# Optimization experiments

Measured on AMD Instinct MI355X. Metric: run time of the kernel, lower is better.

The kernel has to match this reference:

```python
import jax, jax.numpy as jnp
import numpy as np

NUM_HEADS = 8
EPS_OT = 0.05    # self.eps
BETA_T = 1.0     # self.beta_t
N_ITERS = 100    # Sinkhorn max_iter (reference runs all iterations; torch breaks early on convergence)


def setup_inputs() -> dict:
    key = jax.random.key(0)
    ks = jax.random.split(key, 10)
    B, N1, N2 = 16, 256, 576
    dim_t, dim_v, dim_out = 512, 512, 512
    s = 0.02  # conv1d k=1 init scale (stand-in for torch default init)
    f32 = jnp.float32
    return {
        "F_t": jax.random.normal(ks[0], (B, N1, dim_t), f32),
        "F_s": jax.random.normal(ks[1], (B, N2, dim_v), f32),
        # Conv1d(kernel_size=1) weights, squeezed to [out, in]; biases default-on in nn.Conv1d
        "Wq": jax.random.normal(ks[2], (dim_out, dim_t), f32) * s,
        "bq": jnp.zeros((dim_out,), f32),
        "Wk": jax.random.normal(ks[3], (dim_out, dim_v), f32) * s,
        "bk": jnp.zeros((dim_out,), f32),
        "Wv": jax.random.normal(ks[4], (dim_out, dim_v), f32) * s,
        "bv": jnp.zeros((dim_out,), f32),
        "Wp": jax.random.normal(ks[5], (dim_out, dim_out), f32) * s,
        "bp": jnp.zeros((dim_out,), f32),
    }


def sinkhorn_log_exp_sum(C, log_mu, log_nu, eps):
    # C: [BH, N1, N2]; fixed-length log-domain Sinkhorn.
    BH, N1, N2 = C.shape
    u0 = jnp.zeros((BH, N1), C.dtype)
    v0 = jnp.zeros((BH, N2), C.dtype)

    def body(carry, _):
        u, v = carry
        # single K per iteration; both u and v updates use the OLD (u, v), matching torch code
        K = (-C + u[:, :, None] + v[:, None, :]) / eps
        u_new = eps * (log_mu - jax.scipy.special.logsumexp(K, axis=2)) + u
        v_new = eps * (log_nu - jax.scipy.special.logsumexp(K, axis=1)) + v
        return (u_new, v_new), None

    (u, v), _ = jax.lax.scan(jax.checkpoint(body), (u0, v0), None, length=N_ITERS)
    return jnp.exp((-C + u[:, :, None] + v[:, None, :]) / eps)


def _l2norm(x, eps=1e-12):
    return x / jnp.maximum(jnp.linalg.norm(x, axis=-1, keepdims=True), eps)


def reference(F_t, F_s, Wq, bq, Wk, bk, Wv, bv, Wp, bp):
    B, N1, _ = F_t.shape
    N2 = F_s.shape[1]
    H = NUM_HEADS
    dim_out = Wq.shape[0]
    hd = dim_out // H

    # Conv1d(kernel=1) == pointwise linear over channel dim
    q = (F_t @ Wq.T + bq).reshape(B, N1, H, hd)
    k = (F_s @ Wk.T + bk).reshape(B, N2, H, hd)
    v = (F_s @ Wv.T + bv).reshape(B, N2, H, hd)

    q = _l2norm(q)
    k = _l2norm(k)

    sim = jnp.einsum('bnkc,bmkc->bknm', q, k) * BETA_T  # [B,H,N1,N2]
    wdist = (1.0 - sim).reshape(B * H, N1, N2)
    sim_f = sim.reshape(B * H, N1, N2)

    log_mu = jnp.log(jnp.asarray(1.0 / N1 + 1e-8, sim.dtype))
    log_nu = jnp.log(jnp.asarray(1.0 / N2 + 1e-8, sim.dtype))
    T = sinkhorn_log_exp_sum(wdist, log_mu, log_nu, EPS_OT)

    score_map = (N1 * N2 * sim_f * T).reshape(B, H, N1, N2)  # attn_drop = identity (p=0)
    F_t_a = jnp.einsum('bknm,bmkc->bnkc', score_map, v).reshape(B, N1, dim_out)
    F_t_a = F_t_a @ Wp.T + bp
    # torch: F_t_a / F_t_a.norm(dim=-1, keepdim=True)  (plain division, no eps clamp)
    F_t_a = F_t_a / jnp.linalg.norm(F_t_a, axis=-1, keepdims=True)
    return F_t_a  # proj_drop = identity (p=0)
```

## Files before the change

kernel.cpp:

```cpp
#include <hip/hip_runtime.h>
#include <math.h>

#define EPS_OT 0.05f
#define INV_EPS 20.0f

typedef unsigned short ushort_t;
typedef __attribute__((ext_vector_type(8))) short short8;
typedef __attribute__((ext_vector_type(4))) float f32x4;
union Pk { uint4 u; short8 s; };

__device__ __forceinline__ unsigned int f2bf(float f) {
  unsigned int u = __float_as_uint(f);
  return (u + 0x7FFFu + ((u >> 16) & 1u)) >> 16;
}
__device__ __forceinline__ float bf2f(unsigned int u) { return __uint_as_float(u << 16); }

__device__ __forceinline__ void bar_lds() {
  asm volatile("s_waitcnt lgkmcnt(0)" ::: "memory");
  __builtin_amdgcn_s_barrier();
  asm volatile("" ::: "memory");
}

__global__ __launch_bounds__(256) void pack_k(const float* __restrict__ F_t,
                                              const float* __restrict__ F_s,
                                              const float* __restrict__ Wq,
                                              const float* __restrict__ Wk,
                                              const float* __restrict__ Wv,
                                              const float* __restrict__ Wp,
                                              ushort_t* __restrict__ Fth, ushort_t* __restrict__ Ftl,
                                              ushort_t* __restrict__ Fsh, ushort_t* __restrict__ Fsl,
                                              ushort_t* __restrict__ Wqh, ushort_t* __restrict__ Wql,
                                              ushort_t* __restrict__ Wkh, ushort_t* __restrict__ Wkl,
                                              ushort_t* __restrict__ Wvh, ushort_t* __restrict__ Wvl,
                                              ushort_t* __restrict__ Wph) {
  const int blk = blockIdx.x;
  const float* src; ushort_t* dh; ushort_t* dl; size_t off;
  if (blk < 2048)      { src = F_t; dh = Fth; dl = Ftl; off = (size_t)blk * 1024; }
  else if (blk < 6656) { src = F_s; dh = Fsh; dl = Fsl; off = (size_t)(blk - 2048) * 1024; }
  else if (blk < 6912) { src = Wq;  dh = Wqh; dl = Wql; off = (size_t)(blk - 6656) * 1024; }
  else if (blk < 7168) { src = Wk;  dh = Wkh; dl = Wkl; off = (size_t)(blk - 6912) * 1024; }
  else if (blk < 7424) { src = Wv;  dh = Wvh; dl = Wvl; off = (size_t)(blk - 7168) * 1024; }
  else                 { src = Wp;  dh = Wph; dl = nullptr; off = (size_t)(blk - 7424) * 1024; }
  const size_t i = off + (size_t)threadIdx.x * 4;
  float4 f = *(const float4*)(src + i);
  unsigned int h0 = f2bf(f.x), h1 = f2bf(f.y), h2 = f2bf(f.z), h3 = f2bf(f.w);
  uint2 hh; hh.x = h0 | (h1 << 16); hh.y = h2 | (h3 << 16);
  *(uint2*)(dh + i) = hh;
  if (dl) {
    uint2 ll;
    ll.x = f2bf(f.x - bf2f(h0)) | (f2bf(f.y - bf2f(h1)) << 16);
    ll.y = f2bf(f.z - bf2f(h2)) | (f2bf(f.w - bf2f(h3)) << 16);
    *(uint2*)(dl + i) = ll;
  }
}

#define GEMM_HL_BODY()                                                                      \
  f32x4 acc[4] = {};                                                                        \
  for (int k0 = 0; k0 < 512; k0 += 64) {                                                    \
    uint4 a0 = *(const uint4*)(Xp_h + k0), a1 = *(const uint4*)(Xp_h + k0 + 8);             \
    uint4 b0 = *(const uint4*)(Xp_l + k0), b1 = *(const uint4*)(Xp_l + k0 + 8);             \
    uint4 c0 = *(const uint4*)(Wp_h + k0), c1 = *(const uint4*)(Wp_h + k0 + 8);             \
    uint4 d0 = *(const uint4*)(Wp_l + k0), d1 = *(const uint4*)(Wp_l + k0 + 8);             \
    __syncthreads();                                                                        \
    *(uint4*)&Xh[r][cg * 16] = a0; *(uint4*)&Xh[r][cg * 16 + 8] = a1;                       \
    *(uint4*)&Xl[r][cg * 16] = b0; *(uint4*)&Xl[r][cg * 16 + 8] = b1;                       \
    *(uint4*)&Wh[r][cg * 16] = c0; *(uint4*)&Wh[r][cg * 16 + 8] = c1;                       \
    *(uint4*)&Wl[r][cg * 16] = d0; *(uint4*)&Wl[r][cg * 16 + 8] = d1;                       \
    __syncthreads();                                                                        \
    _Pragma("unroll") for (int kst = 0; kst < 2; ++kst) {                                   \
      short8 ah = *(const short8*)&Xh[16 * w + li][kst * 32 + 8 * lg];                      \
      short8 al = *(const short8*)&Xl[16 * w + li][kst * 32 + 8 * lg];                      \
      _Pragma("unroll") for (int nt = 0; nt < 4; ++nt) {                                    \
        short8 bh = *(const short8*)&Wh[nt * 16 + li][kst * 32 + 8 * lg];                   \
        short8 bl = *(const short8*)&Wl[nt * 16 + li][kst * 32 + 8 * lg];                   \
        acc[nt] = __builtin_amdgcn_mfma_f32_16x16x32_bf16(ah, bh, acc[nt], 0, 0, 0);        \
        acc[nt] = __builtin_amdgcn_mfma_f32_16x16x32_bf16(ah, bl, acc[nt], 0, 0, 0);        \
        acc[nt] = __builtin_amdgcn_mfma_f32_16x16x32_bf16(al, bh, acc[nt], 0, 0, 0);        \
      }                                                                                     \
    }                                                                                       \
  }

#define GEMM_PL_BODY()                                                                      \
  f32x4 acc[4] = {};                                                                        \
  for (int k0 = 0; k0 < 512; k0 += 64) {                                                    \
    uint4 a0 = *(const uint4*)(Xp_h + k0), a1 = *(const uint4*)(Xp_h + k0 + 8);             \
    uint4 c0 = *(const uint4*)(Wp_h + k0), c1 = *(const uint4*)(Wp_h + k0 + 8);             \
    __syncthreads();                                                                        \
    *(uint4*)&Xh[r][cg * 16] = a0; *(uint4*)&Xh[r][cg * 16 + 8] = a1;                       \
    *(uint4*)&Wh[r][cg * 16] = c0; *(uint4*)&Wh[r][cg * 16 + 8] = c1;                       \
    __syncthreads();                                                                        \
    _Pragma("unroll") for (int kst = 0; kst < 2; ++kst) {                                   \
      short8 ah = *(const short8*)&Xh[16 * w + li][kst * 32 + 8 * lg];                      \
      _Pragma("unroll") for (int nt = 0; nt < 4; ++nt) {                                    \
        short8 bh = *(const short8*)&Wh[nt * 16 + li][kst * 32 + 8 * lg];                   \
        acc[nt] = __builtin_amdgcn_mfma_f32_16x16x32_bf16(ah, bh, acc[nt], 0, 0, 0);        \
      }                                                                                     \
    }                                                                                       \
  }

__global__ __launch_bounds__(256) void gemmnorm2_k(const ushort_t* __restrict__ Xg_h,
                                                   const ushort_t* __restrict__ Xg_l,
                                                   const ushort_t* __restrict__ Wg_h,
                                                   const ushort_t* __restrict__ Wg_l,
                                                   const float* __restrict__ bias,
                                                   ushort_t* __restrict__ oh,
                                                   ushort_t* __restrict__ ol, int Nn) {
  __shared__ ushort_t Xh[64][72], Xl[64][72], Wh[64][72], Wl[64][72];
  const int tid = threadIdx.x;
  const int w = tid >> 6, l = tid & 63, li = l & 15, lg = l >> 4;
  const int r = tid >> 2, cg = tid & 3;
  const int m0 = blockIdx.x << 6;
  const int h = blockIdx.y, n0 = h << 6;
  const ushort_t* Xp_h = Xg_h + (size_t)(m0 + r) * 512 + cg * 16;
  const ushort_t* Xp_l = Xg_l + (size_t)(m0 + r) * 512 + cg * 16;
  const ushort_t* Wp_h = Wg_h + (size_t)(n0 + r) * 512 + cg * 16;
  const ushort_t* Wp_l = Wg_l + (size_t)(n0 + r) * 512 + cg * 16;
  GEMM_HL_BODY()
  float v[4][4];
  float ss[4] = {0.f, 0.f, 0.f, 0.f};
#pragma unroll
  for (int nt = 0; nt < 4; ++nt) {
    float bb = bias[n0 + nt * 16 + li];
#pragma unroll
    for (int reg = 0; reg < 4; ++reg) {
      float y = acc[nt][reg] + bb;
      v[nt][reg] = y;
      ss[reg] = fmaf(y, y, ss[reg]);
    }
  }
#pragma unroll
  for (int off = 1; off < 16; off <<= 1)
#pragma unroll
    for (int reg = 0; reg < 4; ++reg) ss[reg] += __shfl_xor(ss[reg], off, 64);
  const int b = m0 / Nn;
  const int nbase = m0 - b * Nn;
  const size_t base = ((size_t)(b * 8 + h) * Nn + nbase + 16 * w + 4 * lg) * 64;
#pragma unroll
  for (int reg = 0; reg < 4; ++reg) {
    float inv = 1.0f / fmaxf(sqrtf(ss[reg]), 1e-12f);
#pragma unroll
    for (int nt = 0; nt < 4; ++nt) {
      float y = v[nt][reg] * inv;
      unsigned int hi = f2bf(y);
      size_t idx = base + (size_t)reg * 64 + nt * 16 + li;
      oh[idx] = (ushort_t)hi;
      ol[idx] = (ushort_t)f2bf(y - bf2f(hi));
    }
  }
}

__global__ __launch_bounds__(256) void gemmtrans2_k(const ushort_t* __restrict__ Xg_h,
                                                    const ushort_t* __restrict__ Wg_h,
                                                    const float* __restrict__ bias,
                                                    ushort_t* __restrict__ vt) {
  __shared__ ushort_t Xh[64][72], Wh[64][72];
  __shared__ ushort_t Vs[64 * 73];
  const int tid = threadIdx.x;
  const int w = tid >> 6, l = tid & 63, li = l & 15, lg = l >> 4;
  const int r = tid >> 2, cg = tid & 3;
  const int m0 = blockIdx.x << 6;
  const int h = blockIdx.y, n0 = h << 6;
  const ushort_t* Xp_h = Xg_h + (size_t)(m0 + r) * 512 + cg * 16;
  const ushort_t* Wp_h = Wg_h + (size_t)(n0 + r) * 512 + cg * 16;
  GEMM_PL_BODY()
#pragma unroll
  for (int nt = 0; nt < 4; ++nt) {
    float bb = bias[n0 + nt * 16 + li];
#pragma unroll
    for (int reg = 0; reg < 4; ++reg)
      Vs[(16 * w + 4 * lg + reg) * 73 + nt * 16 + li] = (ushort_t)f2bf(acc[nt][reg] + bb);
  }
  __syncthreads();
  const int a9 = m0 >> 6;
  const int b = a9 / 9;
  const int nbase = m0 - b * 576;
  const int s = b * 8 + h;
  const int c = tid >> 2, q4 = tid & 3;
  ushort_t tmp[16];
#pragma unroll
  for (int jj = 0; jj < 16; ++jj) tmp[jj] = Vs[(q4 * 16 + jj) * 73 + c];
  ushort_t* op = vt + ((size_t)s * 64 + c) * 576 + nbase + q4 * 16;
  *(uint4*)op = *(uint4*)&tmp[0];
  *(uint4*)(op + 8) = *(uint4*)&tmp[8];
}

__global__ __launch_bounds__(256) void gemmplain_k(const ushort_t* __restrict__ Xg_h,
                                                   const ushort_t* __restrict__ Wg_h,
                                                   const float* __restrict__ bias,
                                                   float* __restrict__ Y) {
  __shared__ ushort_t Xh[64][72], Wh[64][72];
  const int tid = threadIdx.x;
  const int w = tid >> 6, l = tid & 63, li = l & 15, lg = l >> 4;
  const int r = tid >> 2, cg = tid & 3;
  const int m0 = blockIdx.x << 6, n0 = blockIdx.y << 6;
  const ushort_t* Xp_h = Xg_h + (size_t)(m0 + r) * 512 + cg * 16;
  const ushort_t* Wp_h = Wg_h + (size_t)(n0 + r) * 512 + cg * 16;
  GEMM_PL_BODY()
#pragma unroll
  for (int nt = 0; nt < 4; ++nt) {
    float bb = bias[n0 + nt * 16 + li];
#pragma unroll
    for (int reg = 0; reg < 4; ++reg)
      Y[(size_t)(m0 + 16 * w + 4 * lg + reg) * 512 + n0 + nt * 16 + li] = acc[nt][reg] + bb;
  }
}

__global__ __launch_bounds__(256) void simE2_k(const ushort_t* __restrict__ qh,
                                               const ushort_t* __restrict__ ql,
                                               const ushort_t* __restrict__ kh,
                                               const ushort_t* __restrict__ kl,
                                               ushort_t* __restrict__ E) {
  const int s = blockIdx.x, i0 = blockIdx.y << 6, j0 = blockIdx.z << 6;
  const int tid = threadIdx.x;
  const int w = tid >> 6, l = tid & 63, li = l & 15, lg = l >> 4;
  const size_t qoff = ((size_t)s * 256 + i0 + 16 * w + li) * 64 + 8 * lg;
  short8 aH0 = *(const short8*)(qh + qoff), aH1 = *(const short8*)(qh + qoff + 32);
  short8 aL0 = *(const short8*)(ql + qoff), aL1 = *(const short8*)(ql + qoff + 32);
  f32x4 acc[4] = {};
#pragma unroll
  for (int nt = 0; nt < 4; ++nt) {
    const size_t koff = ((size_t)s * 576 + j0 + nt * 16 + li) * 64 + 8 * lg;
    short8 bH0 = *(const short8*)(kh + koff), bH1 = *(const short8*)(kh + koff + 32);
    short8 bL0 = *(const short8*)(kl + koff), bL1 = *(const short8*)(kl + koff + 32);
    acc[nt] = __builtin_amdgcn_mfma_f32_16x16x32_bf16(aH0, bH0, acc[nt], 0, 0, 0);
    acc[nt] = __builtin_amdgcn_mfma_f32_16x16x32_bf16(aH1, bH1, acc[nt], 0, 0, 0);
    acc[nt] = __builtin_amdgcn_mfma_f32_16x16x32_bf16(aH0, bL0, acc[nt], 0, 0, 0);
    acc[nt] = __builtin_amdgcn_mfma_f32_16x16x32_bf16(aH1, bL1, acc[nt], 0, 0, 0);
    acc[nt] = __builtin_amdgcn_mfma_f32_16x16x32_bf16(aL0, bH0, acc[nt], 0, 0, 0);
    acc[nt] = __builtin_amdgcn_mfma_f32_16x16x32_bf16(aL1, bH1, acc[nt], 0, 0, 0);
  }
  ushort_t* Ep = E + (size_t)s * 147456;
#pragma unroll
  for (int nt = 0; nt < 4; ++nt)
#pragma unroll
    for (int reg = 0; reg < 4; ++reg) {
      float e = __expf((acc[nt][reg] - 1.0f) * INV_EPS);
      Ep[(size_t)(i0 + 16 * w + 4 * lg + reg) * 576 + j0 + nt * 16 + li] = (ushort_t)f2bf(e);
    }
}

#define SK_SMEM 147456

__global__ __launch_bounds__(1024, 1) void sinkhorn10_k(const ushort_t* __restrict__ E,
                                                        float* __restrict__ gA,
                                                        float* __restrict__ gB,
                                                        unsigned long long* __restrict__ gpart,
                                                        float C_mu, float C_nu) {
  extern __shared__ char smem[];
  const int g = blockIdx.x, s = g >> 1, rh = g & 1, pg = g ^ 1;
  const int tid = threadIdx.x, w = tid >> 6, l = tid & 63, li = l & 15, lg = l >> 4;
  unsigned long long* myP = gpart + (size_t)g * 1152;
  const unsigned long long* prP = gpart + (size_t)pg * 1152;

  ushort_t* Elds = (ushort_t*)smem;
  {
    const uint4* Eg = (const uint4*)(E + (size_t)s * 147456 + (size_t)rh * 73728);
    uint4* El4 = (uint4*)Elds;
    for (int idx = tid; idx < 9216; idx += 1024) El4[idx] = Eg[idx];
  }
  __syncthreads();

  short8 afr[9];
#pragma unroll
  for (int rt = 0; rt < 8; ++rt)
    afr[rt] = *(const short8*)(Elds + (rt * 16 + li) * 576 + w * 32 + 8 * lg);
  const int rtx = w & 7, ktx = 16 + (w >> 3);
  afr[8] = *(const short8*)(Elds + (rtx * 16 + li) * 576 + ktx * 32 + 8 * lg);
  const int ktB = w >> 2, ntb = (w & 3) * 9;
  short8 bfr[9];
#pragma unroll
  for (int p9 = 0; p9 < 9; ++p9) {
    const ushort_t* p = Elds + (ktB * 32 + 8 * lg) * 576 + (ntb + p9) * 16 + li;
    Pk pk;
    pk.u.x = (unsigned int)p[0]    | ((unsigned int)p[576]  << 16);
    pk.u.y = (unsigned int)p[1152] | ((unsigned int)p[1728] << 16);
    pk.u.z = (unsigned int)p[2304] | ((unsigned int)p[2880] << 16);
    pk.u.w = (unsigned int)p[3456] | ((unsigned int)p[4032] << 16);
    bfr[p9] = pk.s;
  }
  __syncthreads();

  float* uu = (float*)smem;
  float* vv = uu + 128;
  ushort_t* au = (ushort_t*)(vv + 576);
  ushort_t* bv = au + 128;
  float* rpart = (float*)(au + 384 + 320);
  float* colp = rpart + 2304;
  float* cso = colp + 2304;

  if (tid < 128) { uu[tid] = 0.0f; au[tid] = (ushort_t)0x3F80; }
  if (tid < 576) { vv[tid] = 0.0f; bv[tid] = (ushort_t)0x3F80; }
  __syncthreads();

  const int jj = tid - 128;
  const bool poller = (tid >= 128) && (tid < 704);

  for (int t = 0; t < 100; ++t) {
    {
      Pk ah; ah.u = *(const uint4*)(au + ktB * 32 + 8 * lg);
      float* cp = colp + ktB * 576;
#pragma unroll
      for (int p9 = 0; p9 < 9; ++p9) {
        f32x4 a2 = {0.f, 0.f, 0.f, 0.f};
        a2 = __builtin_amdgcn_mfma_f32_16x16x32_bf16(ah.s, bfr[p9], a2, 0, 0, 0);
        if (l < 16) cp[(ntb + p9) * 16 + l] = a2[0];
      }
    }
    bar_lds();
    const int par = t & 1;
    if (tid < 576) {
      float cs = colp[tid] + colp[576 + tid] + colp[1152 + tid] + colp[1728 + tid];
      cso[tid] = cs;
      unsigned long long pv = (unsigned long long)__float_as_uint(cs) |
                              ((unsigned long long)(unsigned int)(t + 1) << 32);
      __hip_atomic_store(&myP[par * 576 + tid], pv, __ATOMIC_RELAXED, __HIP_MEMORY_SCOPE_AGENT);
    }
    unsigned long long p0 = 0;
    if (poller)
      p0 = __hip_atomic_load(&prP[par * 576 + jj], __ATOMIC_RELAXED, __HIP_MEMORY_SCOPE_AGENT);
    {
      Pk bh, bhx;
      bh.u = *(const uint4*)(bv + w * 32 + 8 * lg);
      bhx.u = *(const uint4*)(bv + ktx * 32 + 8 * lg);
#pragma unroll
      for (int rt = 0; rt < 8; ++rt) {
        f32x4 a1 = {0.f, 0.f, 0.f, 0.f};
        a1 = __builtin_amdgcn_mfma_f32_16x16x32_bf16(bh.s, afr[rt], a1, 0, 0, 0);
        if (l < 16) rpart[w * 128 + rt * 16 + l] = a1[0];
      }
      f32x4 a1 = {0.f, 0.f, 0.f, 0.f};
      a1 = __builtin_amdgcn_mfma_f32_16x16x32_bf16(bhx.s, afr[8], a1, 0, 0, 0);
      if (l < 16) rpart[ktx * 128 + rtx * 16 + l] = a1[0];
    }
    bar_lds();
    if (tid < 128) {
      float rs = 0.0f;
#pragma unroll
      for (int kc = 0; kc < 18; ++kc) rs += rpart[kc * 128 + tid];
      float un = C_mu - EPS_OT * __logf(rs);
      uu[tid] = un;
      au[tid] = (ushort_t)f2bf(__expf(fminf(fmaxf(un * INV_EPS, -80.f), 80.f)));
    } else if (tid < 704) {
      const unsigned int tg = (unsigned int)(t + 1);
      while ((unsigned int)(p0 >> 32) != tg) {
        __builtin_amdgcn_s_sleep(1);
        p0 = __hip_atomic_load(&prP[par * 576 + jj], __ATOMIC_RELAXED, __HIP_MEMORY_SCOPE_AGENT);
      }
      float tot = cso[jj] + __uint_as_float((unsigned int)p0);
      float vn = C_nu - EPS_OT * __logf(tot);
      vv[jj] = vn;
      bv[jj] = (ushort_t)f2bf(__expf(fminf(fmaxf(vn * INV_EPS, -80.f), 80.f)));
    }
    bar_lds();
  }
  if (tid < 128) gA[(size_t)s * 256 + rh * 128 + tid] = uu[tid] * INV_EPS;
  if (rh == 0 && tid < 576) gB[(size_t)s * 576 + tid] = vv[tid] * INV_EPS + 11.9012851f;
}

__global__ __launch_bounds__(256) void scorev2_k(const ushort_t* __restrict__ E,
                                                 const ushort_t* __restrict__ vt,
                                                 const float* __restrict__ gA,
                                                 const float* __restrict__ gB,
                                                 ushort_t* __restrict__ Y) {
  __shared__ float gBs[576];
  const int s = blockIdx.x, i0 = blockIdx.y << 6;
  const int tid = threadIdx.x;
  const int w = tid >> 6, l = tid & 63, li = l & 15, lg = l >> 4;
  for (int j = tid; j < 576; j += 256) gBs[j] = gB[(size_t)s * 576 + j];
  const float ga = gA[(size_t)s * 256 + i0 + 16 * w + li];
  const ushort_t* Erow = E + (size_t)s * 147456 + (size_t)(i0 + 16 * w + li) * 576;
  f32x4 acc[4] = {};
  __syncthreads();
  for (int kst = 0; kst < 18; ++kst) {
    const int jb = kst * 32 + 8 * lg;
    Pk eu; eu.u = *(const uint4*)(Erow + jb);
    float pv[8];
#pragma unroll
    for (int jj = 0; jj < 8; ++jj) {
      unsigned int us = (unsigned int)(unsigned short)eu.s[jj];
      float e = bf2f(us);
      float le = __logf(e);
      pv[jj] = (1.0f + EPS_OT * le) * __expf(le + ga + gBs[jb + jj]);
    }
    Pk ph, pl;
#pragma unroll
    for (int jj = 0; jj < 8; ++jj) {
      unsigned int h = f2bf(pv[jj]);
      ((unsigned short*)&ph.s)[jj] = (unsigned short)h;
      ((unsigned short*)&pl.s)[jj] = (unsigned short)f2bf(pv[jj] - bf2f(h));
    }
#pragma unroll
    for (int nt = 0; nt < 4; ++nt) {
      Pk vf; vf.u = *(const uint4*)(vt + ((size_t)s * 64 + nt * 16 + li) * 576 + jb);
      acc[nt] = __builtin_amdgcn_mfma_f32_16x16x32_bf16(ph.s, vf.s, acc[nt], 0, 0, 0);
      acc[nt] = __builtin_amdgcn_mfma_f32_16x16x32_bf16(pl.s, vf.s, acc[nt], 0, 0, 0);
    }
  }
  const int b = s >> 3, h = s & 7;
#pragma unroll
  for (int nt = 0; nt < 4; ++nt)
#pragma unroll
    for (int reg = 0; reg < 4; ++reg)
      Y[((size_t)(b * 256 + i0 + 16 * w + 4 * lg + reg) << 9) + (h << 6) + nt * 16 + li] =
          (ushort_t)f2bf(acc[nt][reg]);
}

__global__ __launch_bounds__(256) void rownorm_k(const float* __restrict__ X,
                                                 float* __restrict__ out) {
  const size_t row = blockIdx.x;
  const int tid = threadIdx.x;
  float x0 = X[(row << 9) + tid], x1 = X[(row << 9) + 256 + tid];
  float st = fmaf(x0, x0, x1 * x1);
#pragma unroll
  for (int off = 32; off; off >>= 1) st += __shfl_xor(st, off, 64);
  __shared__ float ps[4];
  if ((tid & 63) == 0) ps[tid >> 6] = st;
  __syncthreads();
  const float inv = 1.0f / sqrtf(ps[0] + ps[1] + ps[2] + ps[3]);
  out[(row << 9) + tid] = x0 * inv;
  out[(row << 9) + 256 + tid] = x1 * inv;
}

extern "C" void kernel_launch(void* const* d_in, const int* in_sizes, int n_in,
                              void* d_out, int out_size, void* d_ws, size_t ws_size,
                              hipStream_t stream) {
  const float* F_t = (const float*)d_in[0];
  const float* F_s = (const float*)d_in[1];
  const float* Wq = (const float*)d_in[2];
  const float* bq = (const float*)d_in[3];
  const float* Wk = (const float*)d_in[4];
  const float* bk = (const float*)d_in[5];
  const float* Wv = (const float*)d_in[6];
  const float* bvb = (const float*)d_in[7];
  const float* Wp = (const float*)d_in[8];
  const float* bp = (const float*)d_in[9];
  float* out = (float*)d_out;

  ushort_t* u0 = (ushort_t*)d_ws;
  ushort_t* Fth = u0;
  ushort_t* Ftl = Fth + 2097152;
  ushort_t* Fsh = Ftl + 2097152;
  ushort_t* Fsl = Fsh + 4718592;
  ushort_t* Wqh = Fsl + 4718592;
  ushort_t* Wql = Wqh + 262144;
  ushort_t* Wkh = Wql + 262144;
  ushort_t* Wkl = Wkh + 262144;
  ushort_t* Wvh = Wkl + 262144;
  ushort_t* Wvl = Wvh + 262144;
  ushort_t* Wph = Wvl + 262144;
  ushort_t* qh = Wph + 262144;
  ushort_t* ql = qh + 2097152;
  ushort_t* kh = ql + 2097152;
  ushort_t* kl = kh + 4718592;
  ushort_t* vt = kl + 4718592;
  ushort_t* Eb = vt + 4718592;
  ushort_t* T0b = Eb + 18874368;
  float* T1 = (float*)(T0b + 2097152);
  float* gA = T1 + 2097152;
  float* gB = gA + 32768;
  unsigned long long* gpart = (unsigned long long*)(gB + 73728);

  const float C_mu = (float)(0.05 * log(1.0 / 256.0 + 1e-8));
  const float C_nu = (float)(0.05 * log(1.0 / 576.0 + 1e-8));

  (void)hipFuncSetAttribute((const void*)sinkhorn10_k,
                            hipFuncAttributeMaxDynamicSharedMemorySize, SK_SMEM);

  pack_k<<<7680, 256, 0, stream>>>(F_t, F_s, Wq, Wk, Wv, Wp, Fth, Ftl, Fsh, Fsl,
                                   Wqh, Wql, Wkh, Wkl, Wvh, Wvl, Wph);
  gemmnorm2_k<<<dim3(64, 8), 256, 0, stream>>>(Fth, Ftl, Wqh, Wql, bq, qh, ql, 256);
  gemmnorm2_k<<<dim3(144, 8), 256, 0, stream>>>(Fsh, Fsl, Wkh, Wkl, bk, kh, kl, 576);
  gemmtrans2_k<<<dim3(144, 8), 256, 0, stream>>>(Fsh, Wvh, bvb, vt);
  simE2_k<<<dim3(128, 4, 9), 256, 0, stream>>>(qh, ql, kh, kl, Eb);
  sinkhorn10_k<<<256, 1024, SK_SMEM, stream>>>(Eb, gA, gB, gpart, C_mu, C_nu);
  scorev2_k<<<dim3(128, 4), 256, 0, stream>>>(Eb, vt, gA, gB, T0b);
  gemmplain_k<<<dim3(64, 8), 256, 0, stream>>>(T0b, Wph, bp, T1);
  rownorm_k<<<4096, 256, 0, stream>>>(T1, out);
}
```

Measured before the change: 408.9 us.

## Restructure Sinkhorn matvec tiling to accumulate K in MFMA and drop a barrier

```diff
diff --git a/kernel.cpp b/kernel.cpp
--- a/kernel.cpp
+++ b/kernel.cpp
@@ -241,7 +241,7 @@
 
 #define SK_SMEM 147456
 
-__global__ __launch_bounds__(1024, 1) void sinkhorn10_k(const ushort_t* __restrict__ E,
+__global__ __launch_bounds__(1024, 1) void sinkhorn11_k(const ushort_t* __restrict__ E,
                                                         float* __restrict__ gA,
                                                         float* __restrict__ gB,
                                                         unsigned long long* __restrict__ gpart,
@@ -260,23 +260,32 @@
   }
   __syncthreads();
 
+  const int art = (w & 7) * 16 + li;
+  const int akb = (w >> 3) * 9;
   short8 afr[9];
 #pragma unroll
-  for (int rt = 0; rt < 8; ++rt)
-    afr[rt] = *(const short8*)(Elds + (rt * 16 + li) * 576 + w * 32 + 8 * lg);
-  const int rtx = w & 7, ktx = 16 + (w >> 3);
-  afr[8] = *(const short8*)(Elds + (rtx * 16 + li) * 576 + ktx * 32 + 8 * lg);
-  const int ktB = w >> 2, ntb = (w & 3) * 9;
-  short8 bfr[9];
-#pragma unroll
-  for (int p9 = 0; p9 < 9; ++p9) {
-    const ushort_t* p = Elds + (ktB * 32 + 8 * lg) * 576 + (ntb + p9) * 16 + li;
-    Pk pk;
-    pk.u.x = (unsigned int)p[0]    | ((unsigned int)p[576]  << 16);
-    pk.u.y = (unsigned int)p[1152] | ((unsigned int)p[1728] << 16);
-    pk.u.z = (unsigned int)p[2304] | ((unsigned int)p[2880] << 16);
-    pk.u.w = (unsigned int)p[3456] | ((unsigned int)p[4032] << 16);
-    bfr[p9] = pk.s;
+  for (int c = 0; c < 9; ++c)
+    afr[c] = *(const short8*)(Elds + art * 576 + (akb + c) * 32 + 8 * lg);
+
+  short8 bfr0, bfr1, bfr2, bfr3, bfr4, bfr5, bfr6, bfr7, bfr8, bfr9, bfr10, bfr11;
+#define BFR_BUILD(dst, tc, q)                                                  \
+  {                                                                            \
+    const ushort_t* p = Elds + ((q) * 32 + 8 * lg) * 576 + (tc) * 16 + li;     \
+    Pk pk;                                                                     \
+    pk.u.x = (unsigned int)p[0]    | ((unsigned int)p[576]  << 16);            \
+    pk.u.y = (unsigned int)p[1152] | ((unsigned int)p[1728] << 16);            \
+    pk.u.z = (unsigned int)p[2304] | ((unsigned int)p[2880] << 16);            \
+    pk.u.w = (unsigned int)p[3456] | ((unsigned int)p[4032] << 16);            \
+    dst = pk.s;                                                                \
+  }
+  BFR_BUILD(bfr0, w, 0) BFR_BUILD(bfr1, w, 1) BFR_BUILD(bfr2, w, 2) BFR_BUILD(bfr3, w, 3)
+  BFR_BUILD(bfr4, w + 16, 0) BFR_BUILD(bfr5, w + 16, 1)
+  BFR_BUILD(bfr6, w + 16, 2) BFR_BUILD(bfr7, w + 16, 3)
+  if (w < 4) {
+    BFR_BUILD(bfr8, w + 32, 0) BFR_BUILD(bfr9, w + 32, 1)
+    BFR_BUILD(bfr10, w + 32, 2) BFR_BUILD(bfr11, w + 32, 3)
+  } else {
+    bfr8 = bfr0; bfr9 = bfr1; bfr10 = bfr2; bfr11 = bfr3;
   }
   __syncthreads();
 
@@ -284,67 +293,66 @@
   float* vv = uu + 128;
   ushort_t* au = (ushort_t*)(vv + 576);
   ushort_t* bv = au + 128;
-  float* rpart = (float*)(au + 384 + 320);
-  float* colp = rpart + 2304;
-  float* cso = colp + 2304;
+  float* rpart = (float*)(au + 768);
+  float* cso = rpart + 256;
 
   if (tid < 128) { uu[tid] = 0.0f; au[tid] = (ushort_t)0x3F80; }
   if (tid < 576) { vv[tid] = 0.0f; bv[tid] = (ushort_t)0x3F80; }
   __syncthreads();
 
   const int jj = tid - 128;
-  const bool poller = (tid >= 128) && (tid < 704);
 
   for (int t = 0; t < 100; ++t) {
+    const int par = t & 1;
     {
-      Pk ah; ah.u = *(const uint4*)(au + ktB * 32 + 8 * lg);
-      float* cp = colp + ktB * 576;
-#pragma unroll
-      for (int p9 = 0; p9 < 9; ++p9) {
-        f32x4 a2 = {0.f, 0.f, 0.f, 0.f};
-        a2 = __builtin_amdgcn_mfma_f32_16x16x32_bf16(ah.s, bfr[p9], a2, 0, 0, 0);
-        if (l < 16) cp[(ntb + p9) * 16 + l] = a2[0];
+      Pk q0, q1, q2, q3;
+      q0.u = *(const uint4*)(au + 8 * lg);
+      q1.u = *(const uint4*)(au + 32 + 8 * lg);
+      q2.u = *(const uint4*)(au + 64 + 8 * lg);
+      q3.u = *(const uint4*)(au + 96 + 8 * lg);
+#define MV2_TILE(tc, f0, f1, f2, f3)                                                  \
+      {                                                                               \
+        f32x4 acc2 = {0.f, 0.f, 0.f, 0.f};                                            \
+        acc2 = __builtin_amdgcn_mfma_f32_16x16x32_bf16(q0.s, f0, acc2, 0, 0, 0);      \
+        acc2 = __builtin_amdgcn_mfma_f32_16x16x32_bf16(q1.s, f1, acc2, 0, 0, 0);      \
+        acc2 = __builtin_amdgcn_mfma_f32_16x16x32_bf16(q2.s, f2, acc2, 0, 0, 0);      \
+        acc2 = __builtin_amdgcn_mfma_f32_16x16x32_bf16(q3.s, f3, acc2, 0, 0, 0);      \
+        if (l < 16) {                                                                 \
+          const int col = (tc) * 16 + l;                                              \
+          float cs = acc2[0];                                                         \
+          cso[col] = cs;                                                              \
+          unsigned long long pv = (unsigned long long)__float_as_uint(cs) |           \
+                                  ((unsigned long long)(unsigned int)(t + 1) << 32);  \
+          __hip_atomic_store(&myP[par * 576 + col], pv, __ATOMIC_RELAXED,             \
+                             __HIP_MEMORY_SCOPE_AGENT);                               \
+        }                                                                             \
       }
-    }
-    bar_lds();
-    const int par = t & 1;
-    if (tid < 576) {
-      float cs = colp[tid] + colp[576 + tid] + colp[1152 + tid] + colp[1728 + tid];
-      cso[tid] = cs;
-      unsigned long long pv = (unsigned long long)__float_as_uint(cs) |
-                              ((unsigned long long)(unsigned int)(t + 1) << 32);
-      __hip_atomic_store(&myP[par * 576 + tid], pv, __ATOMIC_RELAXED, __HIP_MEMORY_SCOPE_AGENT);
-    }
-    unsigned long long p0 = 0;
-    if (poller)
-      p0 = __hip_atomic_load(&prP[par * 576 + jj], __ATOMIC_RELAXED, __HIP_MEMORY_SCOPE_AGENT);
+      MV2_TILE(w, bfr0, bfr1, bfr2, bfr3)
+      MV2_TILE(w + 16, bfr4, bfr5, bfr6, bfr7)
+      if (w < 4) MV2_TILE(w + 32, bfr8, bfr9, bfr10, bfr11)
+    }
     {
-      Pk bh, bhx;
-      bh.u = *(const uint4*)(bv + w * 32 + 8 * lg);
-      bhx.u = *(const uint4*)(bv + ktx * 32 + 8 * lg);
-#pragma unroll
-      for (int rt = 0; rt < 8; ++rt) {
-        f32x4 a1 = {0.f, 0.f, 0.f, 0.f};
-        a1 = __builtin_amdgcn_mfma_f32_16x16x32_bf16(bh.s, afr[rt], a1, 0, 0, 0);
-        if (l < 16) rpart[w * 128 + rt * 16 + l] = a1[0];
+      f32x4 acc1 = {0.f, 0.f, 0.f, 0.f};
+#pragma unroll
+      for (int c = 0; c < 9; ++c) {
+        Pk bh; bh.u = *(const uint4*)(bv + (akb + c) * 32 + 8 * lg);
+        acc1 = __builtin_amdgcn_mfma_f32_16x16x32_bf16(bh.s, afr[c], acc1, 0, 0, 0);
       }
-      f32x4 a1 = {0.f, 0.f, 0.f, 0.f};
-      a1 = __builtin_amdgcn_mfma_f32_16x16x32_bf16(bhx.s, afr[8], a1, 0, 0, 0);
-      if (l < 16) rpart[ktx * 128 + rtx * 16 + l] = a1[0];
+      if (l < 16) rpart[(w >> 3) * 128 + (w & 7) * 16 + l] = acc1[0];
     }
     bar_lds();
     if (tid < 128) {
-      float rs = 0.0f;
-#pragma unroll
-      for (int kc = 0; kc < 18; ++kc) rs += rpart[kc * 128 + tid];
+      float rs = rpart[tid] + rpart[128 + tid];
       float un = C_mu - EPS_OT * __logf(rs);
       uu[tid] = un;
       au[tid] = (ushort_t)f2bf(__expf(fminf(fmaxf(un * INV_EPS, -80.f), 80.f)));
     } else if (tid < 704) {
       const unsigned int tg = (unsigned int)(t + 1);
-      while ((unsigned int)(p0 >> 32) != tg) {
+      unsigned long long p0;
+      for (;;) {
+        p0 = __hip_atomic_load(&prP[par * 576 + jj], __ATOMIC_RELAXED, __HIP_MEMORY_SCOPE_AGENT);
+        if ((unsigned int)(p0 >> 32) == tg) break;
         __builtin_amdgcn_s_sleep(1);
-        p0 = __hip_atomic_load(&prP[par * 576 + jj], __ATOMIC_RELAXED, __HIP_MEMORY_SCOPE_AGENT);
       }
       float tot = cso[jj] + __uint_as_float((unsigned int)p0);
       float vn = C_nu - EPS_OT * __logf(tot);
@@ -353,6 +361,17 @@
     }
     bar_lds();
   }
+  if (rh == 0 && tid >= 128 && tid < 704) {
+    unsigned long long p0;
+    for (;;) {
+      p0 = __hip_atomic_load(&prP[576 + jj], __ATOMIC_RELAXED, __HIP_MEMORY_SCOPE_AGENT);
+      if ((unsigned int)(p0 >> 32) == 100u) break;
+      __builtin_amdgcn_s_sleep(1);
+    }
+    float tot = cso[jj] + __uint_as_float((unsigned int)p0);
+    vv[jj] = C_nu - EPS_OT * __logf(tot);
+  }
+  __syncthreads();
   if (tid < 128) gA[(size_t)s * 256 + rh * 128 + tid] = uu[tid] * INV_EPS;
   if (rh == 0 && tid < 576) gB[(size_t)s * 576 + tid] = vv[tid] * INV_EPS + 11.9012851f;
 }
@@ -463,7 +482,7 @@
   const float C_mu = (float)(0.05 * log(1.0 / 256.0 + 1e-8));
   const float C_nu = (float)(0.05 * log(1.0 / 576.0 + 1e-8));
 
-  (void)hipFuncSetAttribute((const void*)sinkhorn10_k,
+  (void)hipFuncSetAttribute((const void*)sinkhorn11_k,
                             hipFuncAttributeMaxDynamicSharedMemorySize, SK_SMEM);
 
   pack_k<<<7680, 256, 0, stream>>>(F_t, F_s, Wq, Wk, Wv, Wp, Fth, Ftl, Fsh, Fsl,
@@ -472,7 +491,7 @@
   gemmnorm2_k<<<dim3(144, 8), 256, 0, stream>>>(Fsh, Fsl, Wkh, Wkl, bk, kh, kl, 576);
   gemmtrans2_k<<<dim3(144, 8), 256, 0, stream>>>(Fsh, Wvh, bvb, vt);
   simE2_k<<<dim3(128, 4, 9), 256, 0, stream>>>(qh, ql, kh, kl, Eb);
-  sinkhorn10_k<<<256, 1024, SK_SMEM, stream>>>(Eb, gA, gB, gpart, C_mu, C_nu);
+  sinkhorn11_k<<<256, 1024, SK_SMEM, stream>>>(Eb, gA, gB, gpart, C_mu, C_nu);
   scorev2_k<<<dim3(128, 4), 256, 0, stream>>>(Eb, vt, gA, gB, T0b);
   gemmplain_k<<<dim3(64, 8), 256, 0, stream>>>(T0b, Wph, bp, T1);
   rownorm_k<<<4096, 256, 0, stream>>>(T1, out);
```

Result: faster. 371.9 us (-9.0%).
